# Optimization experiments

Measured on AMD Instinct MI355X. Metric: run time of the kernel, lower is better.

## Reference

```python
import jax, jax.numpy as jnp
import numpy as np

V, E, H = 512, 128, 256
B, S, T = 2048, 32, 48


def setup_inputs() -> dict:
    key = jax.random.key(0)
    ks = jax.random.split(key, 13)
    def p(i, shape):
        return jax.random.normal(ks[i], shape, dtype=jnp.float32) * 0.05
    return {
        "source": jax.random.randint(ks[0], (B, S), 0, V),
        "target_len": T,
        "enc_emb": p(1, (V, E)),
        "enc_Wih": p(2, (4 * H, E)),
        "enc_Whh": p(3, (4 * H, H)),
        "enc_bih": p(4, (4 * H,)),
        "enc_bhh": p(5, (4 * H,)),
        "dec_emb": p(6, (V, E)),
        "dec_Wih": p(7, (4 * H, E)),
        "dec_Whh": p(8, (4 * H, H)),
        "dec_bih": p(9, (4 * H,)),
        "dec_bhh": p(10, (4 * H,)),
        "fc_W": p(11, (V, H)),
        "fc_b": p(12, (V,)),
    }


def lstm_cell(x, h, c, Wih, Whh, bih, bhh):
    # torch gate order: i, f, g, o
    z = x @ Wih.T + h @ Whh.T + (bih + bhh)
    i, f, g, o = jnp.split(z, 4, axis=-1)
    c = jax.nn.sigmoid(f) * c + jax.nn.sigmoid(i) * jnp.tanh(g)
    h = jax.nn.sigmoid(o) * jnp.tanh(c)
    return h, c


def reference(source, target_len, enc_emb, enc_Wih, enc_Whh, enc_bih, enc_bhh,
              dec_emb, dec_Wih, dec_Whh, dec_bih, dec_bhh, fc_W, fc_b):
    Bsz = source.shape[0]
    Hd = enc_Whh.shape[1]
    h0 = jnp.zeros((Bsz, Hd), dtype=enc_emb.dtype)
    c0 = jnp.zeros((Bsz, Hd), dtype=enc_emb.dtype)

    # ---- encoder: embed whole source, scan single-layer LSTM over time ----
    emb_seq = jnp.swapaxes(enc_emb[source], 0, 1)  # [S, B, E]

    def enc_step(carry, x_t):
        h, c = carry
        h, c = lstm_cell(x_t, h, c, enc_Wih, enc_Whh, enc_bih, enc_bhh)
        return (h, c), None

    (h, c), _ = jax.lax.scan(enc_step, (h0, c0), emb_seq)

    sos = jnp.zeros((Bsz,), dtype=jnp.int32)  # char2idx.get('<SOS>', 0) == 0

    def dec_step(carry, _):
        tok, h, c = carry
        x = dec_emb[tok]                         # [B, E]
        h, c = lstm_cell(x, h, c, dec_Wih, dec_Whh, dec_bih, dec_bhh)
        logits = h @ fc_W.T + fc_b               # [B, V]
        nxt = jnp.argmax(logits, axis=-1).astype(jnp.int32)
        return (nxt, h, c), logits

    _, logits = jax.lax.scan(dec_step, (sos, h, c), None, length=target_len)
    return jnp.swapaxes(logits, 0, 1)            # [B, target_len, V]
```

## Files before the change

kernel.cpp:

```cpp
#include <hip/hip_runtime.h>
#include <cmath>

#define S_LEN 32
#define E_DIM 128
#define H_DIM 256
#define V_DIM 512
#define NTILE 18
#define W_TILES 12
#define TILE_SHORTS 8192
#define A_SHORTS 12288
#define ZPITCH 132

typedef _Float16 f16x8v __attribute__((ext_vector_type(8)));
typedef float f32x16 __attribute__((ext_vector_type(16)));

#define SCALE_S 4096.0f
#define INV_S   2.44140625e-4f

__device__ __forceinline__ float sigf(float x) { return 1.0f / (1.0f + expf(-x)); }

template<int L>
__device__ __forceinline__ unsigned short lvl_f16(float x) {
  _Float16 h1 = (_Float16)x;
  if (L == 1) return __builtin_bit_cast(unsigned short, h1);
  _Float16 h2 = (_Float16)((x - (float)h1) * SCALE_S);
  return __builtin_bit_cast(unsigned short, h2);
}

__global__ void prep_weights(const float* __restrict__ eWih, const float* __restrict__ eWhh,
                             const float* __restrict__ dWih, const float* __restrict__ dWhh,
                             unsigned short* __restrict__ We, unsigned short* __restrict__ Wd,
                             float* __restrict__ h0, float* __restrict__ c,
                             int* __restrict__ tok)
{
  const int b = blockIdx.x;
  if (b >= 192) {
    const int pb = b - 192;
    const int gt = pb * 256 + threadIdx.x;
    float4 z = make_float4(0.f, 0.f, 0.f, 0.f);
    float4* p0 = (float4*)h0;
    float4* pc = (float4*)c;
    for (int i = gt; i < 131072; i += 16384) { p0[i] = z; pc[i] = z; }
    if (gt < 2048) tok[gt] = 0;
    return;
  }
  const int j    = b % W_TILES;
  const int rest = b / W_TILES;
  const int nb   = rest & 7;
  const int set  = rest >> 3;
  const float* Wih = set ? dWih : eWih;
  const float* Whh = set ? dWhh : eWhh;
  unsigned short* dst = (set ? Wd : We) + ((size_t)nb * W_TILES + j) * TILE_SHORTS;
  const int lvl = (j < 6) ? 1 : 2;
  const int jj  = (j < 6) ? j : j - 6;

  for (int cpos = threadIdx.x; cpos < 1024; cpos += 256) {
    int fi = cpos >> 6, l = cpos & 63;
    int g = fi >> 2, kc = fi & 3;
    int n  = g * H_DIM + nb * 32 + (l & 31);
    int kk = jj * 64 + kc * 16 + (l >> 5) * 8;
    unsigned short o8[8];
    #pragma unroll
    for (int e = 0; e < 8; ++e) {
      int k = kk + e;
      float v = (k < E_DIM) ? Wih[(size_t)n * E_DIM + k]
                            : Whh[(size_t)n * H_DIM + (k - E_DIM)];
      o8[e] = (lvl == 1) ? lvl_f16<1>(v) : lvl_f16<2>(v);
    }
    uint4 pk;
    pk.x = (unsigned)o8[0] | ((unsigned)o8[1] << 16);
    pk.y = (unsigned)o8[2] | ((unsigned)o8[3] << 16);
    pk.z = (unsigned)o8[4] | ((unsigned)o8[5] << 16);
    pk.w = (unsigned)o8[6] | ((unsigned)o8[7] << 16);
    *(uint4*)&dst[(size_t)cpos * 8] = pk;
  }
}

__device__ __forceinline__ void stage_A12(unsigned short* Ax1, unsigned short* Ax2,
                                          const float* __restrict__ esrc,
                                          const float* __restrict__ hsrc,
                                          int arow, int q8) {
  #pragma unroll
  for (int j = 0; j < 12; ++j) {
    int k0, kA;
    const float* src;
    if (j < 4) { kA = q8 * 4 + 32 * j;            src = esrc + kA; }
    else       { k0 = q8 * 4 + 32 * (j - 4); kA = E_DIM + k0; src = hsrc + k0; }
    float4 v = *(const float4*)src;
    _Float16 a1x = (_Float16)v.x, a1y = (_Float16)v.y,
             a1z = (_Float16)v.z, a1w = (_Float16)v.w;
    _Float16 a2x = (_Float16)((v.x - (float)a1x) * SCALE_S);
    _Float16 a2y = (_Float16)((v.y - (float)a1y) * SCALE_S);
    _Float16 a2z = (_Float16)((v.z - (float)a1z) * SCALE_S);
    _Float16 a2w = (_Float16)((v.w - (float)a1w) * SCALE_S);
    int lane_w = arow + ((kA >> 3) & 1) * 32;
    int idx = (((kA >> 4)) * 64 + lane_w) * 8 + (kA & 7);
    uint2 p1, p2;
    p1.x = (unsigned)__builtin_bit_cast(unsigned short, a1x)
         | ((unsigned)__builtin_bit_cast(unsigned short, a1y) << 16);
    p1.y = (unsigned)__builtin_bit_cast(unsigned short, a1z)
         | ((unsigned)__builtin_bit_cast(unsigned short, a1w) << 16);
    p2.x = (unsigned)__builtin_bit_cast(unsigned short, a2x)
         | ((unsigned)__builtin_bit_cast(unsigned short, a2y) << 16);
    p2.y = (unsigned)__builtin_bit_cast(unsigned short, a2z)
         | ((unsigned)__builtin_bit_cast(unsigned short, a2w) << 16);
    *(uint2*)&Ax1[idx] = p1;
    *(uint2*)&Ax2[idx] = p2;
  }
}

__launch_bounds__(256, 2)
__global__ void lstm_mfma_kernel(const float* __restrict__ emb,
                                 const int* __restrict__ idx_src, int idx_stride, int idx_off,
                                 const unsigned short* __restrict__ Wf,
                                 const float* __restrict__ bih, const float* __restrict__ bhh,
                                 const float* __restrict__ h_in,
                                 float* __restrict__ h_out, float* __restrict__ c)
{
  __shared__ __align__(16) unsigned short smem[2 * A_SHORTS];
  unsigned short* Ax1 = smem;
  unsigned short* Ax2 = smem + A_SHORTS;

  const int tid  = threadIdx.x;
  const int lane = tid & 63;
  const int w    = tid >> 6;
  const int m0 = blockIdx.x * 32;
  const int nb = blockIdx.y;
  const int nc0 = nb * 32;

  const int arow = tid >> 3;
  const int q8   = tid & 7;
  const int token = idx_src[(size_t)(m0 + arow) * idx_stride + idx_off];
  const float* esrc = emb + (size_t)token * E_DIM;
  const float* hsrc = h_in + (size_t)(m0 + arow) * H_DIM;

  const int col32 = lane & 31;
  const int lhi   = lane >> 5;

  const unsigned short* wbase = Wf + (size_t)nb * (W_TILES * TILE_SHORTS)
                                   + (size_t)(w * 4) * 512 + (size_t)lane * 8;

  f32x16 accA, accB;
  #pragma unroll
  for (int r = 0; r < 16; ++r) { accA[r] = 0.f; accB[r] = 0.f; }

  uint4 pA[4], pB[4], pC[4], pD[4];

#define LOADT(J, P)                                                            \
  {                                                                            \
    const unsigned short* bsrc =                                               \
        wbase + (size_t)(((J) < W_TILES) ? (J) : (J) - W_TILES) * TILE_SHORTS; \
    _Pragma("unroll")                                                          \
    for (int kc = 0; kc < 4; ++kc) P[kc] = *(const uint4*)(bsrc + (size_t)kc * 512); \
  }

#define MFMAT(J, P, ACCX, AXB)                                                 \
  {                                                                            \
    const int jj = ((J) < 6) ? (J) : (((J) < 12) ? (J) - 6 : (J) - 12);        \
    _Pragma("unroll")                                                          \
    for (int kc = 0; kc < 4; ++kc) {                                           \
      f16x8v af = *(const f16x8v*)&AXB[(jj * 4 + kc) * 512 + lane * 8];        \
      f16x8v bfr = __builtin_bit_cast(f16x8v, P[kc]);                          \
      ACCX = __builtin_amdgcn_mfma_f32_32x32x16_f16(af, bfr, ACCX, 0, 0, 0);   \
    }                                                                          \
  }

  LOADT(0, pA); LOADT(1, pB); LOADT(2, pC);

  stage_A12(Ax1, Ax2, esrc, hsrc, arow, q8);
  asm volatile("s_waitcnt lgkmcnt(0)" ::: "memory");
  __builtin_amdgcn_s_barrier();

  LOADT(3, pD);  MFMAT(0, pA, accA, Ax1);
  LOADT(4, pA);  MFMAT(1, pB, accA, Ax1);
  LOADT(5, pB);  MFMAT(2, pC, accA, Ax1);
  LOADT(6, pC);  MFMAT(3, pD, accA, Ax1);
  LOADT(7, pD);  MFMAT(4, pA, accA, Ax1);
  LOADT(8, pA);  MFMAT(5, pB, accA, Ax1);
  LOADT(9, pB);  MFMAT(6, pC, accB, Ax1);
  LOADT(10, pC); MFMAT(7, pD, accB, Ax1);
  LOADT(11, pD); MFMAT(8, pA, accB, Ax1);
  LOADT(12, pA); MFMAT(9, pB, accB, Ax1);
  LOADT(13, pB); MFMAT(10, pC, accB, Ax1);
  LOADT(14, pC); MFMAT(11, pD, accB, Ax1);
  LOADT(15, pD); MFMAT(12, pA, accB, Ax2);
  LOADT(16, pA); MFMAT(13, pB, accB, Ax2);
  LOADT(17, pB); MFMAT(14, pC, accB, Ax2);

  const int er = tid >> 3;
  const int ec = tid & 7;
  const float* cp0 = c + (size_t)(m0 + er) * H_DIM + nc0 + ec * 4;
  float4 cold = *(const float4*)(cp0);

  MFMAT(15, pD, accB, Ax2);
  MFMAT(16, pA, accB, Ax2);
  MFMAT(17, pB, accB, Ax2);

#undef LOADT
#undef MFMAT

  const float bsv = bih[w * H_DIM + nc0 + col32] + bhh[w * H_DIM + nc0 + col32];

  float* zb = (float*)smem;
  asm volatile("s_waitcnt lgkmcnt(0)" ::: "memory");
  __builtin_amdgcn_s_barrier();

  #pragma unroll
  for (int r = 0; r < 16; ++r) {
    int row_l = (r & 3) + 8 * (r >> 2) + 4 * lhi;
    zb[row_l * ZPITCH + col32 * 4 + w] = fmaf(accB[r], INV_S, accA[r]) + bsv;
  }

  asm volatile("s_waitcnt lgkmcnt(0)" ::: "memory");
  __builtin_amdgcn_s_barrier();

  {
    float* hp  = h_out + (size_t)(m0 + er) * H_DIM + nc0 + ec * 4;
    float* cpw = (float*)cp0;
    float cov[4] = {cold.x, cold.y, cold.z, cold.w};
    float cnv[4], hnv[4];
    #pragma unroll
    for (int cc = 0; cc < 4; ++cc) {
      float4 zq = *(const float4*)&zb[er * ZPITCH + (ec * 4 + cc) * 4];
      float zi = zq.x, zf = zq.y, zg = zq.z, zo = zq.w;
      float cn = sigf(zf) * cov[cc] + sigf(zi) * tanhf(zg);
      cnv[cc] = cn;
      hnv[cc] = sigf(zo) * tanhf(cn);
    }
    *(float4*)cpw = make_float4(cnv[0], cnv[1], cnv[2], cnv[3]);
    *(float4*)hp  = make_float4(hnv[0], hnv[1], hnv[2], hnv[3]);
  }
}

__launch_bounds__(256)
__global__ void declog_kernel(const float* __restrict__ h,
                              const float* __restrict__ fcW,
                              const float* __restrict__ fcb,
                              float* __restrict__ out,
                              int* __restrict__ tok,
                              int t, int T)
{
  __shared__ float bv[8][256];
  __shared__ int   bi[8][256];

  const int tid  = threadIdx.x;
  const int lane = tid & 63;
  const int wv   = tid >> 6;
  const int r0   = blockIdx.x * 8;
  const int c0   = tid * 2;

  const float* hb  = h + (size_t)r0 * H_DIM;
  const float* w0p = fcW + (size_t)c0 * H_DIM;
  const float* w1p = w0p + H_DIM;

  float acc[8][2] = {};

  #pragma unroll 1
  for (int k0 = 0; k0 < H_DIM; k0 += 16) {
    float4 b0[4], b1[4];
    #pragma unroll
    for (int q = 0; q < 4; ++q) {
      b0[q] = *(const float4*)(w0p + k0 + q * 4);
      b1[q] = *(const float4*)(w1p + k0 + q * 4);
    }
    #pragma unroll
    for (int q = 0; q < 4; ++q) {
      #pragma unroll
      for (int r = 0; r < 8; ++r) {
        float4 a = *(const float4*)(hb + (size_t)r * H_DIM + k0 + q * 4);
        acc[r][0] = fmaf(a.x, b0[q].x, acc[r][0]);
        acc[r][0] = fmaf(a.y, b0[q].y, acc[r][0]);
        acc[r][0] = fmaf(a.z, b0[q].z, acc[r][0]);
        acc[r][0] = fmaf(a.w, b0[q].w, acc[r][0]);
        acc[r][1] = fmaf(a.x, b1[q].x, acc[r][1]);
        acc[r][1] = fmaf(a.y, b1[q].y, acc[r][1]);
        acc[r][1] = fmaf(a.z, b1[q].z, acc[r][1]);
        acc[r][1] = fmaf(a.w, b1[q].w, acc[r][1]);
      }
    }
  }

  const float fb0 = fcb[c0];
  const float fb1 = fcb[c0 + 1];
  #pragma unroll
  for (int r = 0; r < 8; ++r) {
    float z0 = acc[r][0] + fb0;
    float z1 = acc[r][1] + fb1;
    *(float2*)(out + (size_t)(r0 + r) * T * V_DIM + (size_t)t * V_DIM + c0)
        = make_float2(z0, z1);
    float v = z0; int ix = c0;
    if (z1 > v) { v = z1; ix = c0 + 1; }
    bv[r][tid] = v;
    bi[r][tid] = ix;
  }
  __syncthreads();

  #pragma unroll
  for (int rr = 0; rr < 2; ++rr) {
    int r = wv * 2 + rr;
    float best = bv[r][lane];
    int   bidx = bi[r][lane];
    #pragma unroll
    for (int s = 1; s < 4; ++s) {
      float ov = bv[r][lane + 64 * s];
      int   oi = bi[r][lane + 64 * s];
      if (ov > best || (ov == best && oi < bidx)) { best = ov; bidx = oi; }
    }
    #pragma unroll
    for (int off = 32; off; off >>= 1) {
      float ov = __shfl_xor(best, off);
      int   oi = __shfl_xor(bidx, off);
      if (ov > best || (ov == best && oi < bidx)) { best = ov; bidx = oi; }
    }
    if (lane == 0) tok[r0 + r] = bidx;
  }
}

extern "C" void kernel_launch(void* const* d_in, const int* in_sizes, int n_in,
                              void* d_out, int out_size, void* d_ws, size_t ws_size,
                              hipStream_t stream) {
  const int*   source  = (const int*)d_in[0];
  const float* enc_emb = (const float*)d_in[2];
  const float* enc_Wih = (const float*)d_in[3];
  const float* enc_Whh = (const float*)d_in[4];
  const float* enc_bih = (const float*)d_in[5];
  const float* enc_bhh = (const float*)d_in[6];
  const float* dec_emb = (const float*)d_in[7];
  const float* dec_Wih = (const float*)d_in[8];
  const float* dec_Whh = (const float*)d_in[9];
  const float* dec_bih = (const float*)d_in[10];
  const float* dec_bhh = (const float*)d_in[11];
  const float* fc_W    = (const float*)d_in[12];
  const float* fc_b    = (const float*)d_in[13];
  float* out = (float*)d_out;

  const int B = in_sizes[0] / S_LEN;
  const int T = out_size / (B * V_DIM);

  const size_t BH = (size_t)B * H_DIM;
  const size_t WFSZ = (size_t)8 * W_TILES * TILE_SHORTS;
  float* h0  = (float*)d_ws;
  float* h1  = h0 + BH;
  float* c   = h1 + BH;
  int*   tok = (int*)(c + BH);
  unsigned short* We = (unsigned short*)(tok + B);
  unsigned short* Wd = We + WFSZ;

  prep_weights<<<dim3(192 + 64), dim3(256), 0, stream>>>(
      enc_Wih, enc_Whh, dec_Wih, dec_Whh, We, Wd, h0, c, tok);

  dim3 blk(256);
  dim3 g_lstm(B / 32, H_DIM / 32);
  dim3 g_declog(B / 8);

  const float* hin = h0;
  float* hout = h1;

  for (int s = 0; s < S_LEN; ++s) {
    lstm_mfma_kernel<<<g_lstm, blk, 0, stream>>>(
        enc_emb, source, S_LEN, s, We, enc_bih, enc_bhh, hin, hout, c);
    const float* tmp = hout; hout = (float*)hin; hin = tmp;
  }

  for (int t = 0; t < T; ++t) {
    lstm_mfma_kernel<<<g_lstm, blk, 0, stream>>>(
        dec_emb, tok, 1, 0, Wd, dec_bih, dec_bhh, hin, hout, c);
    const float* tmp = hout; hout = (float*)hin; hin = tmp;
    declog_kernel<<<g_declog, blk, 0, stream>>>(hin, fc_W, fc_b, out, tok, t, T);
  }
}
```

Measured before the change: 1.777 ms.

## Precompute embedding-times-Wih tables and drop input projection from LSTM GEMM

Because the input to each LSTM step is an embedding row, emb @ Wih^T is precomputed once per vocabulary entry for the encoder and the decoder in the prep kernel. Each step kernel then only runs the recurrent h @ Whh^T MFMA and adds a gathered fp32 row of the table during the gate epilogue. This cuts the K dimension from 384 to 256, shrinking weight tiles, MFMA count and LDS staging. The cost is a one-time V×4H projection per weight set plus an extra gathered global read per step. The input projection is now exact fp32 rather than split-f16.

```diff
diff --git a/kernel.cpp b/kernel.cpp
--- a/kernel.cpp
+++ b/kernel.cpp
@@ -5,10 +5,10 @@
 #define E_DIM 128
 #define H_DIM 256
 #define V_DIM 512
-#define NTILE 18
-#define W_TILES 12
+#define NTILE 12
+#define W_TILES 8
 #define TILE_SHORTS 8192
-#define A_SHORTS 12288
+#define A_SHORTS 8192
 #define ZPITCH 132
 
 typedef _Float16 f16x8v __attribute__((ext_vector_type(8)));
@@ -27,15 +27,17 @@
   return __builtin_bit_cast(unsigned short, h2);
 }
 
-__global__ void prep_weights(const float* __restrict__ eWih, const float* __restrict__ eWhh,
+__global__ void prep_weights(const float* __restrict__ eemb, const float* __restrict__ demb,
+                             const float* __restrict__ eWih, const float* __restrict__ eWhh,
                              const float* __restrict__ dWih, const float* __restrict__ dWhh,
                              unsigned short* __restrict__ We, unsigned short* __restrict__ Wd,
+                             float* __restrict__ PE, float* __restrict__ PD,
                              float* __restrict__ h0, float* __restrict__ c,
                              int* __restrict__ tok)
 {
   const int b = blockIdx.x;
-  if (b >= 192) {
-    const int pb = b - 192;
+  if (b >= 1152) {
+    const int pb = b - 1152;
     const int gt = pb * 256 + threadIdx.x;
     float4 z = make_float4(0.f, 0.f, 0.f, 0.f);
     float4* p0 = (float4*)h0;
@@ -44,15 +46,38 @@
     if (gt < 2048) tok[gt] = 0;
     return;
   }
+  if (b >= 128) {
+    const int pb  = b - 128;
+    const int set = pb >> 9;
+    const int v   = pb & 511;
+    const float* Wih  = set ? dWih : eWih;
+    const float* embr = (set ? demb : eemb) + (size_t)v * E_DIM;
+    float* dst = (set ? PD : PE) + (size_t)v * 1024;
+    const int n0 = threadIdx.x * 4;
+    float acc[4] = {0.f, 0.f, 0.f, 0.f};
+    #pragma unroll 4
+    for (int k0 = 0; k0 < E_DIM; k0 += 4) {
+      float4 e = *(const float4*)(embr + k0);
+      #pragma unroll
+      for (int i = 0; i < 4; ++i) {
+        float4 wv = *(const float4*)(Wih + (size_t)(n0 + i) * E_DIM + k0);
+        acc[i] = fmaf(e.x, wv.x, acc[i]);
+        acc[i] = fmaf(e.y, wv.y, acc[i]);
+        acc[i] = fmaf(e.z, wv.z, acc[i]);
+        acc[i] = fmaf(e.w, wv.w, acc[i]);
+      }
+    }
+    *(float4*)(dst + n0) = make_float4(acc[0], acc[1], acc[2], acc[3]);
+    return;
+  }
   const int j    = b % W_TILES;
   const int rest = b / W_TILES;
   const int nb   = rest & 7;
   const int set  = rest >> 3;
-  const float* Wih = set ? dWih : eWih;
   const float* Whh = set ? dWhh : eWhh;
   unsigned short* dst = (set ? Wd : We) + ((size_t)nb * W_TILES + j) * TILE_SHORTS;
-  const int lvl = (j < 6) ? 1 : 2;
-  const int jj  = (j < 6) ? j : j - 6;
+  const int lvl = (j < 4) ? 1 : 2;
+  const int jj  = j & 3;
 
   for (int cpos = threadIdx.x; cpos < 1024; cpos += 256) {
     int fi = cpos >> 6, l = cpos & 63;
@@ -62,9 +87,7 @@
     unsigned short o8[8];
     #pragma unroll
     for (int e = 0; e < 8; ++e) {
-      int k = kk + e;
-      float v = (k < E_DIM) ? Wih[(size_t)n * E_DIM + k]
-                            : Whh[(size_t)n * H_DIM + (k - E_DIM)];
+      float v = Whh[(size_t)n * H_DIM + kk + e];
       o8[e] = (lvl == 1) ? lvl_f16<1>(v) : lvl_f16<2>(v);
     }
     uint4 pk;
@@ -77,16 +100,12 @@
 }
 
 __device__ __forceinline__ void stage_A12(unsigned short* Ax1, unsigned short* Ax2,
-                                          const float* __restrict__ esrc,
                                           const float* __restrict__ hsrc,
                                           int arow, int q8) {
   #pragma unroll
-  for (int j = 0; j < 12; ++j) {
-    int k0, kA;
-    const float* src;
-    if (j < 4) { kA = q8 * 4 + 32 * j;            src = esrc + kA; }
-    else       { k0 = q8 * 4 + 32 * (j - 4); kA = E_DIM + k0; src = hsrc + k0; }
-    float4 v = *(const float4*)src;
+  for (int j = 0; j < 8; ++j) {
+    int kA = q8 * 4 + 32 * j;
+    float4 v = *(const float4*)(hsrc + kA);
     _Float16 a1x = (_Float16)v.x, a1y = (_Float16)v.y,
              a1z = (_Float16)v.z, a1w = (_Float16)v.w;
     _Float16 a2x = (_Float16)((v.x - (float)a1x) * SCALE_S);
@@ -94,7 +113,7 @@
     _Float16 a2z = (_Float16)((v.z - (float)a1z) * SCALE_S);
     _Float16 a2w = (_Float16)((v.w - (float)a1w) * SCALE_S);
     int lane_w = arow + ((kA >> 3) & 1) * 32;
-    int idx = (((kA >> 4)) * 64 + lane_w) * 8 + (kA & 7);
+    int idx = ((kA >> 4) * 64 + lane_w) * 8 + (kA & 7);
     uint2 p1, p2;
     p1.x = (unsigned)__builtin_bit_cast(unsigned short, a1x)
          | ((unsigned)__builtin_bit_cast(unsigned short, a1y) << 16);
@@ -110,7 +129,7 @@
 }
 
 __launch_bounds__(256, 2)
-__global__ void lstm_mfma_kernel(const float* __restrict__ emb,
+__global__ void lstm_mfma_kernel(const float* __restrict__ pcomp,
                                  const int* __restrict__ idx_src, int idx_stride, int idx_off,
                                  const unsigned short* __restrict__ Wf,
                                  const float* __restrict__ bih, const float* __restrict__ bhh,
@@ -131,7 +150,6 @@
   const int arow = tid >> 3;
   const int q8   = tid & 7;
   const int token = idx_src[(size_t)(m0 + arow) * idx_stride + idx_off];
-  const float* esrc = emb + (size_t)token * E_DIM;
   const float* hsrc = h_in + (size_t)(m0 + arow) * H_DIM;
 
   const int col32 = lane & 31;
@@ -148,18 +166,16 @@
 
 #define LOADT(J, P)                                                            \
   {                                                                            \
-    const unsigned short* bsrc =                                               \
-        wbase + (size_t)(((J) < W_TILES) ? (J) : (J) - W_TILES) * TILE_SHORTS; \
+    const unsigned short* bsrc = wbase + (size_t)((J) & 7) * TILE_SHORTS;      \
     _Pragma("unroll")                                                          \
     for (int kc = 0; kc < 4; ++kc) P[kc] = *(const uint4*)(bsrc + (size_t)kc * 512); \
   }
 
 #define MFMAT(J, P, ACCX, AXB)                                                 \
   {                                                                            \
-    const int jj = ((J) < 6) ? (J) : (((J) < 12) ? (J) - 6 : (J) - 12);        \
     _Pragma("unroll")                                                          \
     for (int kc = 0; kc < 4; ++kc) {                                           \
-      f16x8v af = *(const f16x8v*)&AXB[(jj * 4 + kc) * 512 + lane * 8];        \
+      f16x8v af = *(const f16x8v*)&AXB[(((J) & 3) * 4 + kc) * 512 + lane * 8]; \
       f16x8v bfr = __builtin_bit_cast(f16x8v, P[kc]);                          \
       ACCX = __builtin_amdgcn_mfma_f32_32x32x16_f16(af, bfr, ACCX, 0, 0, 0);   \
     }                                                                          \
@@ -167,7 +183,7 @@
 
   LOADT(0, pA); LOADT(1, pB); LOADT(2, pC);
 
-  stage_A12(Ax1, Ax2, esrc, hsrc, arow, q8);
+  stage_A12(Ax1, Ax2, hsrc, arow, q8);
   asm volatile("s_waitcnt lgkmcnt(0)" ::: "memory");
   __builtin_amdgcn_s_barrier();
 
@@ -175,26 +191,27 @@
   LOADT(4, pA);  MFMAT(1, pB, accA, Ax1);
   LOADT(5, pB);  MFMAT(2, pC, accA, Ax1);
   LOADT(6, pC);  MFMAT(3, pD, accA, Ax1);
-  LOADT(7, pD);  MFMAT(4, pA, accA, Ax1);
-  LOADT(8, pA);  MFMAT(5, pB, accA, Ax1);
+  LOADT(7, pD);  MFMAT(4, pA, accB, Ax1);
+  LOADT(8, pA);  MFMAT(5, pB, accB, Ax1);
   LOADT(9, pB);  MFMAT(6, pC, accB, Ax1);
   LOADT(10, pC); MFMAT(7, pD, accB, Ax1);
-  LOADT(11, pD); MFMAT(8, pA, accB, Ax1);
-  LOADT(12, pA); MFMAT(9, pB, accB, Ax1);
-  LOADT(13, pB); MFMAT(10, pC, accB, Ax1);
-  LOADT(14, pC); MFMAT(11, pD, accB, Ax1);
-  LOADT(15, pD); MFMAT(12, pA, accB, Ax2);
-  LOADT(16, pA); MFMAT(13, pB, accB, Ax2);
-  LOADT(17, pB); MFMAT(14, pC, accB, Ax2);
-
-  const int er = tid >> 3;
-  const int ec = tid & 7;
+  LOADT(11, pD); MFMAT(8, pA, accB, Ax2);
+
+  const int er = arow;
+  const int ec = q8;
   const float* cp0 = c + (size_t)(m0 + er) * H_DIM + nc0 + ec * 4;
   float4 cold = *(const float4*)(cp0);
-
-  MFMAT(15, pD, accB, Ax2);
-  MFMAT(16, pA, accB, Ax2);
-  MFMAT(17, pB, accB, Ax2);
+  const float* pxr = pcomp + (size_t)token * 1024 + nc0 + ec * 4;
+  float pxa[4][4];
+  #pragma unroll
+  for (int g = 0; g < 4; ++g) {
+    float4 t = *(const float4*)(pxr + g * H_DIM);
+    pxa[g][0] = t.x; pxa[g][1] = t.y; pxa[g][2] = t.z; pxa[g][3] = t.w;
+  }
+
+  MFMAT(9, pB, accB, Ax2);
+  MFMAT(10, pC, accB, Ax2);
+  MFMAT(11, pD, accB, Ax2);
 
 #undef LOADT
 #undef MFMAT
@@ -222,7 +239,10 @@
     #pragma unroll
     for (int cc = 0; cc < 4; ++cc) {
       float4 zq = *(const float4*)&zb[er * ZPITCH + (ec * 4 + cc) * 4];
-      float zi = zq.x, zf = zq.y, zg = zq.z, zo = zq.w;
+      float zi = zq.x + pxa[0][cc];
+      float zf = zq.y + pxa[1][cc];
+      float zg = zq.z + pxa[2][cc];
+      float zo = zq.w + pxa[3][cc];
       float cn = sigf(zf) * cov[cc] + sigf(zi) * tanhf(zg);
       cnv[cc] = cn;
       hnv[cc] = sigf(zo) * tanhf(cn);
@@ -345,9 +365,12 @@
   int*   tok = (int*)(c + BH);
   unsigned short* We = (unsigned short*)(tok + B);
   unsigned short* Wd = We + WFSZ;
-
-  prep_weights<<<dim3(192 + 64), dim3(256), 0, stream>>>(
-      enc_Wih, enc_Whh, dec_Wih, dec_Whh, We, Wd, h0, c, tok);
+  float* PE = (float*)(Wd + WFSZ);
+  float* PD = PE + (size_t)V_DIM * 1024;
+
+  prep_weights<<<dim3(128 + 1024 + 64), dim3(256), 0, stream>>>(
+      enc_emb, dec_emb, enc_Wih, enc_Whh, dec_Wih, dec_Whh,
+      We, Wd, PE, PD, h0, c, tok);
 
   dim3 blk(256);
   dim3 g_lstm(B / 32, H_DIM / 32);
@@ -358,13 +381,13 @@
 
   for (int s = 0; s < S_LEN; ++s) {
     lstm_mfma_kernel<<<g_lstm, blk, 0, stream>>>(
-        enc_emb, source, S_LEN, s, We, enc_bih, enc_bhh, hin, hout, c);
+        PE, source, S_LEN, s, We, enc_bih, enc_bhh, hin, hout, c);
     const float* tmp = hout; hout = (float*)hin; hin = tmp;
   }
 
   for (int t = 0; t < T; ++t) {
     lstm_mfma_kernel<<<g_lstm, blk, 0, stream>>>(
-        dec_emb, tok, 1, 0, Wd, dec_bih, dec_bhh, hin, hout, c);
+        PD, tok, 1, 0, Wd, dec_bih, dec_bhh, hin, hout, c);
     const float* tmp = hout; hout = (float*)hin; hin = tmp;
     declog_kernel<<<g_declog, blk, 0, stream>>>(hin, fc_W, fc_b, out, tok, t, T);
   }
```

Result: faster. 1.679 ms, median of 2 (-5.6%).
